# Kernel optimization log

Measured on AMD Instinct MI355X. Metric: run time of the kernel, lower is better.

The kernel has to match this reference:

```python
import jax, jax.numpy as jnp
import numpy as np

TEMPERATURE = 8.0  # sqrt(d_k) with d_k = 64
EPS = 1e-8


def setup_inputs() -> dict:
    key = jax.random.key(0)
    kq, kk, kv, km = jax.random.split(key, 4)
    B, L, D = 16, 2048, 64
    q = jax.random.normal(kq, (B, L, D), dtype=jnp.float32)
    k = jax.random.normal(kk, (B, L, D), dtype=jnp.float32)
    v = jax.random.normal(kv, (B, L, D), dtype=jnp.float32)
    # True entries are zeroed out AFTER softmax (post-softmax masking)
    mask = jax.random.randint(km, (B, L, L), 0, 2).astype(jnp.bool_)
    return {"q": q, "k": k, "v": v, "mask": mask}


def reference(q, k, v, mask):
    # attn scores: [B, Lq, Lk]
    attn = jnp.einsum("bqd,bkd->bqk", q, k) / TEMPERATURE
    attn = jax.nn.softmax(attn, axis=2)
    # post-softmax masking followed by renormalization (breaks flash-attn fusion)
    attn = jnp.where(mask, 0.0, attn)
    attn = attn / (jnp.sum(attn, axis=2, keepdims=True) + EPS)
    # dropout is identity in eval/reference mode
    output = jnp.einsum("bqk,bkd->bqd", attn, v)
    return output, attn
```

## Files before the change

kernel.cpp:

```cpp
#include <hip/hip_runtime.h>

#define BATCH 16
#define LSEQ 2048
#define DIM 64
#define TQ 32
#define SSTRIDE 2056
#define EPSV 1e-8f
#define SCALE_LOG2E 0.18033688011112042f

typedef float f4 __attribute__((ext_vector_type(4)));
typedef _Float16 h4 __attribute__((ext_vector_type(4)));
typedef _Float16 h8 __attribute__((ext_vector_type(8)));
typedef int i4t __attribute__((ext_vector_type(4)));

__device__ inline h8 cvt_h8(f4 a, f4 b) {
    h8 r;
    r[0] = (_Float16)a[0]; r[1] = (_Float16)a[1];
    r[2] = (_Float16)a[2]; r[3] = (_Float16)a[3];
    r[4] = (_Float16)b[0]; r[5] = (_Float16)b[1];
    r[6] = (_Float16)b[2]; r[7] = (_Float16)b[3];
    return r;
}

__device__ inline float fast_exp2(float x) {
#if __has_builtin(__builtin_amdgcn_exp2f)
    return __builtin_amdgcn_exp2f(x);
#else
    return exp2f(x);
#endif
}

__device__ inline void lds_barrier() {
    asm volatile("s_waitcnt lgkmcnt(0)" ::: "memory");
    __builtin_amdgcn_s_barrier();
    __builtin_amdgcn_sched_barrier(0);
}

__global__ __launch_bounds__(256)
void cvt_k_kernel(const float* __restrict__ k, _Float16* __restrict__ kh) {
    const int idx = blockIdx.x * 256 + threadIdx.x;
    f4 v = ((const f4*)k)[idx];
    h4 h;
    #pragma unroll
    for (int e = 0; e < 4; ++e) h[e] = (_Float16)v[e];
    ((h4*)kh)[idx] = h;
}

__global__ __launch_bounds__(256)
void tr_v_kernel(const float* __restrict__ v, _Float16* __restrict__ vt) {
    __shared__ float tile[64][65];
    const int b = blockIdx.y, k0 = blockIdx.x * 64, t = threadIdx.x;
    const float* vb = v + ((size_t)b * LSEQ + k0) * DIM;
    #pragma unroll
    for (int p = 0; p < 4; ++p) {
        const int row = p * 16 + (t >> 4), c4 = (t & 15) * 4;
        f4 val = *(const f4*)(vb + row * DIM + c4);
        #pragma unroll
        for (int e = 0; e < 4; ++e) tile[row][c4 + e] = val[e];
    }
    __syncthreads();
    _Float16* vtb = vt + (size_t)b * DIM * LSEQ;
    #pragma unroll
    for (int p = 0; p < 4; ++p) {
        const int d = p * 16 + (t >> 4), k4 = (t & 15) * 4;
        h4 h;
        #pragma unroll
        for (int e = 0; e < 4; ++e) h[e] = (_Float16)tile[k4 + e][d];
        *(h4*)(vtb + (size_t)d * LSEQ + k0 + k4) = h;
    }
}

__global__ __launch_bounds__(1024, 4)
void attn_kernel(const float* __restrict__ q, const _Float16* __restrict__ kh,
                 const _Float16* __restrict__ vt, const int* __restrict__ mask,
                 float* __restrict__ out, float* __restrict__ attn)
{
    __shared__ __align__(16) _Float16 s_p[TQ][SSTRIDE];
    __shared__ float oacc[16][256];
    __shared__ float s_inv[TQ];

    const int b    = blockIdx.y;
    const int q0   = blockIdx.x * TQ;
    const int tid  = threadIdx.x;
    const int w    = tid >> 6;
    const int lane = tid & 63;
    const int quad = lane >> 4;
    const int m16  = lane & 15;

    const int* mrow0 = mask + ((size_t)b * LSEQ + q0 + 2 * w) * LSEQ;
    i4t mv0[8];
    #pragma unroll
    for (int j = 0; j < 8; ++j)
        mv0[j] = __builtin_nontemporal_load((const i4t*)(mrow0 + lane * 4 + 256 * j));

    const float* qrowA = q + ((size_t)b * LSEQ + q0 + m16) * DIM + quad * 8;
    const float* qrowB = qrowA + 16 * DIM;
    h8 aqA0 = cvt_h8(*(const f4*)(qrowA),      *(const f4*)(qrowA + 4));
    h8 aqA1 = cvt_h8(*(const f4*)(qrowA + 32), *(const f4*)(qrowA + 36));
    h8 aqB0 = cvt_h8(*(const f4*)(qrowB),      *(const f4*)(qrowB + 4));
    h8 aqB1 = cvt_h8(*(const f4*)(qrowB + 32), *(const f4*)(qrowB + 36));

    #pragma unroll 2
    for (int i = 0; i < 8; ++i) {
        const int c = w * 16 + i * 256;
        const _Float16* krow = kh + ((size_t)b * LSEQ + c + m16) * DIM + quad * 8;
        h8 bk0 = *(const h8*)(krow);
        h8 bk1 = *(const h8*)(krow + 32);
        f4 accA = {0.f, 0.f, 0.f, 0.f}, accB = {0.f, 0.f, 0.f, 0.f};
        accA = __builtin_amdgcn_mfma_f32_16x16x32_f16(aqA0, bk0, accA, 0, 0, 0);
        accA = __builtin_amdgcn_mfma_f32_16x16x32_f16(aqA1, bk1, accA, 0, 0, 0);
        accB = __builtin_amdgcn_mfma_f32_16x16x32_f16(aqB0, bk0, accB, 0, 0, 0);
        accB = __builtin_amdgcn_mfma_f32_16x16x32_f16(aqB1, bk1, accB, 0, 0, 0);
        #pragma unroll
        for (int r = 0; r < 4; ++r) {
            s_p[quad * 4 + r][c + m16]      = (_Float16)(accA[r] * SCALE_LOG2E);
            s_p[16 + quad * 4 + r][c + m16] = (_Float16)(accB[r] * SCALE_LOG2E);
        }
    }

    const int* mrow1 = mrow0 + LSEQ;
    i4t mv1[8];
    #pragma unroll
    for (int j = 0; j < 8; ++j)
        mv1[j] = __builtin_nontemporal_load((const i4t*)(mrow1 + lane * 4 + 256 * j));

    lds_barrier();

    float inv0 = 0.f, inv1 = 0.f;
    #pragma unroll
    for (int rr = 0; rr < 2; ++rr) {
        const int row = 2 * w + rr;
        float sa = 0.f, sk = 0.f;
        h4 pk[8];
        #pragma unroll
        for (int j = 0; j < 8; ++j) {
            h4 hv = *(const h4*)(&s_p[row][lane * 4 + 256 * j]);
            i4t m = rr ? mv1[j] : mv0[j];
            #pragma unroll
            for (int e = 0; e < 4; ++e) {
                float p = fast_exp2((float)hv[e]);
                sa += p;
                float pm = m[e] ? 0.f : p;
                sk += pm;
                pk[j][e] = (_Float16)pm;
            }
        }
        #pragma unroll
        for (int off = 32; off >= 1; off >>= 1) {
            sa += __shfl_xor(sa, off);
            sk += __shfl_xor(sk, off);
        }
        const float inv_d = 1.f / (sk + EPSV * sa);
        if (rr == 0) inv0 = inv_d; else inv1 = inv_d;
        if (lane == 0) s_inv[row] = inv_d;
        #pragma unroll
        for (int j = 0; j < 8; ++j)
            *(h4*)(&s_p[row][lane * 4 + 256 * j]) = pk[j];
    }

    lds_barrier();

    const int dt = w & 3;
    const int kq = w >> 2;
    const _Float16* vtr = vt + ((size_t)b * DIM + dt * 16 + m16) * LSEQ;
    f4 accA = {0.f, 0.f, 0.f, 0.f}, accB = {0.f, 0.f, 0.f, 0.f};
    #pragma unroll 4
    for (int kb = kq * 512; kb < kq * 512 + 512; kb += 32) {
        const int kk = kb + quad * 8;
        h8 bf  = *(const h8*)(vtr + kk);
        h8 afA = *(const h8*)(&s_p[m16][kk]);
        h8 afB = *(const h8*)(&s_p[16 + m16][kk]);
        accA = __builtin_amdgcn_mfma_f32_16x16x32_f16(afA, bf, accA, 0, 0, 0);
        accB = __builtin_amdgcn_mfma_f32_16x16x32_f16(afB, bf, accB, 0, 0, 0);
    }

    #pragma unroll
    for (int rr = 0; rr < 2; ++rr) {
        const int row = 2 * w + rr;
        const float ivd = rr ? inv1 : inv0;
        float* arow = attn + ((size_t)b * LSEQ + q0 + row) * LSEQ;
        #pragma unroll
        for (int j = 0; j < 8; ++j) {
            const int c = lane * 4 + 256 * j;
            h4 hv = *(const h4*)(&s_p[row][c]);
            f4 pv;
            #pragma unroll
            for (int e = 0; e < 4; ++e) pv[e] = ivd * (float)hv[e];
            __builtin_nontemporal_store(pv, (f4*)(&arow[c]));
        }
    }

    float* ob = out + ((size_t)b * LSEQ + q0) * DIM;

    #pragma unroll
    for (int r = 0; r < 4; ++r)
        oacc[w][(quad * 4 + r) * 16 + m16] = accA[r];
    lds_barrier();
    {
        const int row = tid >> 6;
        const int d   = tid & 63;
        const int dt2 = d >> 4, dc = d & 15;
        const int o   = row * 16 + dc;
        float vsum = oacc[dt2][o] + oacc[4 + dt2][o]
                   + oacc[8 + dt2][o] + oacc[12 + dt2][o];
        ob[row * DIM + d] = s_inv[row] * vsum;
    }
    lds_barrier();

    #pragma unroll
    for (int r = 0; r < 4; ++r)
        oacc[w][(quad * 4 + r) * 16 + m16] = accB[r];
    lds_barrier();
    {
        const int row = tid >> 6;
        const int d   = tid & 63;
        const int dt2 = d >> 4, dc = d & 15;
        const int o   = row * 16 + dc;
        float vsum = oacc[dt2][o] + oacc[4 + dt2][o]
                   + oacc[8 + dt2][o] + oacc[12 + dt2][o];
        ob[(16 + row) * DIM + d] = s_inv[16 + row] * vsum;
    }
}

__global__ __launch_bounds__(512, 4)
void attn_kernel_fb(const float* __restrict__ q, const float* __restrict__ k,
                    const float* __restrict__ v, const int* __restrict__ mask,
                    float* __restrict__ out, float* __restrict__ attn)
{
    __shared__ __align__(16) _Float16 s_p[16][SSTRIDE];
    __shared__ float oacc[8][16 * 16];
    __shared__ float s_inv[16];

    const int b = blockIdx.y, q0 = blockIdx.x * 16, tid = threadIdx.x;
    const int w = tid >> 6, lane = tid & 63, quad = lane >> 4, m16 = lane & 15;
    const float* kp = k + (size_t)b * LSEQ * DIM;
    const float* vp = v + (size_t)b * LSEQ * DIM;
    const float* qrow = q + ((size_t)b * LSEQ + q0 + m16) * DIM + quad * 8;
    h8 aq0 = cvt_h8(*(const f4*)(qrow),      *(const f4*)(qrow + 4));
    h8 aq1 = cvt_h8(*(const f4*)(qrow + 32), *(const f4*)(qrow + 36));

    for (int t = w; t < LSEQ / 16; t += 8) {
        const int c = t * 16;
        const float* krow = kp + (size_t)(c + m16) * DIM + quad * 8;
        h8 bk0 = cvt_h8(*(const f4*)(krow),      *(const f4*)(krow + 4));
        h8 bk1 = cvt_h8(*(const f4*)(krow + 32), *(const f4*)(krow + 36));
        f4 acc = {0.f, 0.f, 0.f, 0.f};
        acc = __builtin_amdgcn_mfma_f32_16x16x32_f16(aq0, bk0, acc, 0, 0, 0);
        acc = __builtin_amdgcn_mfma_f32_16x16x32_f16(aq1, bk1, acc, 0, 0, 0);
        #pragma unroll
        for (int r = 0; r < 4; ++r)
            s_p[quad * 4 + r][c + m16] = (_Float16)(acc[r] * 0.125f);
    }
    __syncthreads();

    #pragma unroll
    for (int rr = 0; rr < 2; ++rr) {
        const int row = 2 * w + rr;
        const int* mrow = mask + ((size_t)b * LSEQ + q0 + row) * LSEQ;
        i4t mv[8];
        #pragma unroll
        for (int j = 0; j < 8; ++j)
            mv[j] = __builtin_nontemporal_load((const i4t*)(mrow + lane * 4 + 256 * j));
        float sa = 0.f, sk = 0.f;
        h4 pk[8];
        #pragma unroll
        for (int j = 0; j < 8; ++j) {
            h4 hv = *(const h4*)(&s_p[row][lane * 4 + 256 * j]);
            #pragma unroll
            for (int e = 0; e < 4; ++e) {
                float p = __expf((float)hv[e]);
                sa += p;
                float pm = mv[j][e] ? 0.f : p;
                sk += pm;
                pk[j][e] = (_Float16)pm;
            }
        }
        #pragma unroll
        for (int off = 32; off >= 1; off >>= 1) {
            sa += __shfl_xor(sa, off);
            sk += __shfl_xor(sk, off);
        }
        const float inv_d = 1.f / (sk + EPSV * sa);
        if (lane == 0) s_inv[row] = inv_d;
        float* arow = attn + ((size_t)b * LSEQ + q0 + row) * LSEQ;
        #pragma unroll
        for (int j = 0; j < 8; ++j) {
            const int c = lane * 4 + 256 * j;
            *(h4*)(&s_p[row][c]) = pk[j];
            f4 pv;
            #pragma unroll
            for (int e = 0; e < 4; ++e) pv[e] = inv_d * (float)pk[j][e];
            __builtin_nontemporal_store(pv, (f4*)(&arow[c]));
        }
    }
    __syncthreads();

    {
        const int dt = w >> 1, kh_ = w & 1;
        f4 acc = {0.f, 0.f, 0.f, 0.f};
        for (int kb0 = kh_ * 1024; kb0 < kh_ * 1024 + 1024; kb0 += 32) {
            const int kk = kb0 + quad * 8;
            h8 af = *(const h8*)(&s_p[m16][kk]);
            const float* vcol = vp + (size_t)kk * DIM + dt * 16 + m16;
            h8 bf;
            #pragma unroll
            for (int j = 0; j < 8; ++j) bf[j] = (_Float16)vcol[j * DIM];
            acc = __builtin_amdgcn_mfma_f32_16x16x32_f16(af, bf, acc, 0, 0, 0);
        }
        #pragma unroll
        for (int r = 0; r < 4; ++r)
            oacc[w][(quad * 4 + r) * 16 + m16] = acc[r];
    }
    __syncthreads();

    float* ob = out + ((size_t)b * LSEQ + q0) * DIM;
    #pragma unroll
    for (int it = 0; it < 2; ++it) {
        const int idx = tid + it * 512;
        const int row = idx >> 6, d = idx & 63;
        const int dt2 = d >> 4, dc = d & 15;
        ob[row * DIM + d] = s_inv[row] *
            (oacc[2 * dt2][row * 16 + dc] + oacc[2 * dt2 + 1][row * 16 + dc]);
    }
}

extern "C" void kernel_launch(void* const* d_in, const int* in_sizes, int n_in,
                              void* d_out, int out_size, void* d_ws, size_t ws_size,
                              hipStream_t stream) {
    const float* q = (const float*)d_in[0];
    const float* k = (const float*)d_in[1];
    const float* v = (const float*)d_in[2];
    const int* mask = (const int*)d_in[3];
    float* out = (float*)d_out;
    float* attn = out + (size_t)BATCH * LSEQ * DIM;

    const size_t kv_elems = (size_t)BATCH * LSEQ * DIM;
    if (ws_size >= kv_elems * 2 * sizeof(_Float16)) {
        _Float16* kh = (_Float16*)d_ws;
        _Float16* vt = kh + kv_elems;
        cvt_k_kernel<<<kv_elems / 4 / 256, 256, 0, stream>>>(k, kh);
        tr_v_kernel<<<dim3(LSEQ / 64, BATCH), 256, 0, stream>>>(v, vt);
        attn_kernel<<<dim3(LSEQ / TQ, BATCH), 1024, 0, stream>>>(q, kh, vt, mask, out, attn);
    } else {
        attn_kernel_fb<<<dim3(LSEQ / 16, BATCH), 512, 0, stream>>>(q, k, v, mask, out, attn);
    }
}
```

Baseline: 499.7 us.

## Process four query tiles per block with mask/Q prefetch; fuse K/V prep kernels

The attention kernel now loops over four consecutive 32-row query tiles per block. The grid shrinks to a quarter of its former size, so there is about one block per CU. While the PV MFMA loop and the attn-row stores for the current tile run, the next tile's mask rows and Q fragments are loaded into registers, so global mask latency overlaps with compute and stores. The K fp16 conversion and the V transpose are merged into one prep kernel to remove a launch. The risk is less parallelism to hide latency, since there are fewer blocks and the loop is serial, and higher register pressure from the prefetched mask arrays.

```diff
diff --git a/kernel.cpp b/kernel.cpp
--- a/kernel.cpp
+++ b/kernel.cpp
@@ -37,19 +37,24 @@
 }
 
 __global__ __launch_bounds__(256)
-void cvt_k_kernel(const float* __restrict__ k, _Float16* __restrict__ kh) {
-    const int idx = blockIdx.x * 256 + threadIdx.x;
-    f4 v = ((const f4*)k)[idx];
-    h4 h;
-    #pragma unroll
-    for (int e = 0; e < 4; ++e) h[e] = (_Float16)v[e];
-    ((h4*)kh)[idx] = h;
-}
-
-__global__ __launch_bounds__(256)
-void tr_v_kernel(const float* __restrict__ v, _Float16* __restrict__ vt) {
+void prep_kernel(const float* __restrict__ k, const float* __restrict__ v,
+                 _Float16* __restrict__ kh, _Float16* __restrict__ vt) {
     __shared__ float tile[64][65];
     const int b = blockIdx.y, k0 = blockIdx.x * 64, t = threadIdx.x;
+
+    {
+        const f4* kb = (const f4*)(k + ((size_t)b * LSEQ + k0) * DIM);
+        h4* khb = (h4*)(kh + ((size_t)b * LSEQ + k0) * DIM);
+        #pragma unroll
+        for (int p = 0; p < 4; ++p) {
+            f4 val = kb[t + 256 * p];
+            h4 h;
+            #pragma unroll
+            for (int e = 0; e < 4; ++e) h[e] = (_Float16)val[e];
+            khb[t + 256 * p] = h;
+        }
+    }
+
     const float* vb = v + ((size_t)b * LSEQ + k0) * DIM;
     #pragma unroll
     for (int p = 0; p < 4; ++p) {
@@ -80,145 +85,168 @@
     __shared__ float s_inv[TQ];
 
     const int b    = blockIdx.y;
-    const int q0   = blockIdx.x * TQ;
     const int tid  = threadIdx.x;
     const int w    = tid >> 6;
     const int lane = tid & 63;
     const int quad = lane >> 4;
     const int m16  = lane & 15;
 
-    const int* mrow0 = mask + ((size_t)b * LSEQ + q0 + 2 * w) * LSEQ;
-    i4t mv0[8];
-    #pragma unroll
-    for (int j = 0; j < 8; ++j)
-        mv0[j] = __builtin_nontemporal_load((const i4t*)(mrow0 + lane * 4 + 256 * j));
-
-    const float* qrowA = q + ((size_t)b * LSEQ + q0 + m16) * DIM + quad * 8;
-    const float* qrowB = qrowA + 16 * DIM;
-    h8 aqA0 = cvt_h8(*(const f4*)(qrowA),      *(const f4*)(qrowA + 4));
-    h8 aqA1 = cvt_h8(*(const f4*)(qrowA + 32), *(const f4*)(qrowA + 36));
-    h8 aqB0 = cvt_h8(*(const f4*)(qrowB),      *(const f4*)(qrowB + 4));
-    h8 aqB1 = cvt_h8(*(const f4*)(qrowB + 32), *(const f4*)(qrowB + 36));
-
-    #pragma unroll 2
-    for (int i = 0; i < 8; ++i) {
-        const int c = w * 16 + i * 256;
-        const _Float16* krow = kh + ((size_t)b * LSEQ + c + m16) * DIM + quad * 8;
-        h8 bk0 = *(const h8*)(krow);
-        h8 bk1 = *(const h8*)(krow + 32);
-        f4 accA = {0.f, 0.f, 0.f, 0.f}, accB = {0.f, 0.f, 0.f, 0.f};
-        accA = __builtin_amdgcn_mfma_f32_16x16x32_f16(aqA0, bk0, accA, 0, 0, 0);
-        accA = __builtin_amdgcn_mfma_f32_16x16x32_f16(aqA1, bk1, accA, 0, 0, 0);
-        accB = __builtin_amdgcn_mfma_f32_16x16x32_f16(aqB0, bk0, accB, 0, 0, 0);
-        accB = __builtin_amdgcn_mfma_f32_16x16x32_f16(aqB1, bk1, accB, 0, 0, 0);
-        #pragma unroll
-        for (int r = 0; r < 4; ++r) {
-            s_p[quad * 4 + r][c + m16]      = (_Float16)(accA[r] * SCALE_LOG2E);
-            s_p[16 + quad * 4 + r][c + m16] = (_Float16)(accB[r] * SCALE_LOG2E);
-        }
-    }
-
-    const int* mrow1 = mrow0 + LSEQ;
-    i4t mv1[8];
-    #pragma unroll
-    for (int j = 0; j < 8; ++j)
-        mv1[j] = __builtin_nontemporal_load((const i4t*)(mrow1 + lane * 4 + 256 * j));
-
-    lds_barrier();
-
-    float inv0 = 0.f, inv1 = 0.f;
-    #pragma unroll
-    for (int rr = 0; rr < 2; ++rr) {
-        const int row = 2 * w + rr;
-        float sa = 0.f, sk = 0.f;
-        h4 pk[8];
+    const _Float16* khb   = kh   + (size_t)b * LSEQ * DIM;
+    const _Float16* vtb   = vt   + (size_t)b * DIM * LSEQ;
+    const int*      mb    = mask + (size_t)b * LSEQ * LSEQ;
+    const float*    qb    = q    + (size_t)b * LSEQ * DIM;
+    float*          outb  = out  + (size_t)b * LSEQ * DIM;
+    float*          attnb = attn + (size_t)b * LSEQ * LSEQ;
+
+    int q0 = blockIdx.x * (4 * TQ);
+
+    i4t mv0[8], mv1[8];
+    {
+        const int* mr0 = mb + (size_t)(q0 + 2 * w) * LSEQ + lane * 4;
+        const int* mr1 = mr0 + LSEQ;
         #pragma unroll
         for (int j = 0; j < 8; ++j) {
-            h4 hv = *(const h4*)(&s_p[row][lane * 4 + 256 * j]);
-            i4t m = rr ? mv1[j] : mv0[j];
-            #pragma unroll
-            for (int e = 0; e < 4; ++e) {
-                float p = fast_exp2((float)hv[e]);
-                sa += p;
-                float pm = m[e] ? 0.f : p;
-                sk += pm;
-                pk[j][e] = (_Float16)pm;
-            }
-        }
-        #pragma unroll
-        for (int off = 32; off >= 1; off >>= 1) {
-            sa += __shfl_xor(sa, off);
-            sk += __shfl_xor(sk, off);
-        }
-        const float inv_d = 1.f / (sk + EPSV * sa);
-        if (rr == 0) inv0 = inv_d; else inv1 = inv_d;
-        if (lane == 0) s_inv[row] = inv_d;
-        #pragma unroll
-        for (int j = 0; j < 8; ++j)
-            *(h4*)(&s_p[row][lane * 4 + 256 * j]) = pk[j];
-    }
-
-    lds_barrier();
-
-    const int dt = w & 3;
-    const int kq = w >> 2;
-    const _Float16* vtr = vt + ((size_t)b * DIM + dt * 16 + m16) * LSEQ;
-    f4 accA = {0.f, 0.f, 0.f, 0.f}, accB = {0.f, 0.f, 0.f, 0.f};
-    #pragma unroll 4
-    for (int kb = kq * 512; kb < kq * 512 + 512; kb += 32) {
-        const int kk = kb + quad * 8;
-        h8 bf  = *(const h8*)(vtr + kk);
-        h8 afA = *(const h8*)(&s_p[m16][kk]);
-        h8 afB = *(const h8*)(&s_p[16 + m16][kk]);
-        accA = __builtin_amdgcn_mfma_f32_16x16x32_f16(afA, bf, accA, 0, 0, 0);
-        accB = __builtin_amdgcn_mfma_f32_16x16x32_f16(afB, bf, accB, 0, 0, 0);
-    }
-
-    #pragma unroll
-    for (int rr = 0; rr < 2; ++rr) {
-        const int row = 2 * w + rr;
-        const float ivd = rr ? inv1 : inv0;
-        float* arow = attn + ((size_t)b * LSEQ + q0 + row) * LSEQ;
-        #pragma unroll
-        for (int j = 0; j < 8; ++j) {
-            const int c = lane * 4 + 256 * j;
-            h4 hv = *(const h4*)(&s_p[row][c]);
-            f4 pv;
-            #pragma unroll
-            for (int e = 0; e < 4; ++e) pv[e] = ivd * (float)hv[e];
-            __builtin_nontemporal_store(pv, (f4*)(&arow[c]));
-        }
-    }
-
-    float* ob = out + ((size_t)b * LSEQ + q0) * DIM;
-
-    #pragma unroll
-    for (int r = 0; r < 4; ++r)
-        oacc[w][(quad * 4 + r) * 16 + m16] = accA[r];
-    lds_barrier();
+            mv0[j] = __builtin_nontemporal_load((const i4t*)(mr0 + 256 * j));
+            mv1[j] = __builtin_nontemporal_load((const i4t*)(mr1 + 256 * j));
+        }
+    }
+    h8 aqA0, aqA1, aqB0, aqB1;
     {
-        const int row = tid >> 6;
-        const int d   = tid & 63;
-        const int dt2 = d >> 4, dc = d & 15;
-        const int o   = row * 16 + dc;
-        float vsum = oacc[dt2][o] + oacc[4 + dt2][o]
-                   + oacc[8 + dt2][o] + oacc[12 + dt2][o];
-        ob[row * DIM + d] = s_inv[row] * vsum;
-    }
-    lds_barrier();
-
-    #pragma unroll
-    for (int r = 0; r < 4; ++r)
-        oacc[w][(quad * 4 + r) * 16 + m16] = accB[r];
-    lds_barrier();
-    {
-        const int row = tid >> 6;
-        const int d   = tid & 63;
-        const int dt2 = d >> 4, dc = d & 15;
-        const int o   = row * 16 + dc;
-        float vsum = oacc[dt2][o] + oacc[4 + dt2][o]
-                   + oacc[8 + dt2][o] + oacc[12 + dt2][o];
-        ob[(16 + row) * DIM + d] = s_inv[16 + row] * vsum;
+        const float* qrowA = qb + (size_t)(q0 + m16) * DIM + quad * 8;
+        const float* qrowB = qrowA + 16 * DIM;
+        aqA0 = cvt_h8(*(const f4*)(qrowA),      *(const f4*)(qrowA + 4));
+        aqA1 = cvt_h8(*(const f4*)(qrowA + 32), *(const f4*)(qrowA + 36));
+        aqB0 = cvt_h8(*(const f4*)(qrowB),      *(const f4*)(qrowB + 4));
+        aqB1 = cvt_h8(*(const f4*)(qrowB + 32), *(const f4*)(qrowB + 36));
+    }
+
+    for (int it = 0; it < 4; ++it, q0 += TQ) {
+        #pragma unroll 2
+        for (int i = 0; i < 8; ++i) {
+            const int c = w * 16 + i * 256;
+            const _Float16* krow = khb + (size_t)(c + m16) * DIM + quad * 8;
+            h8 bk0 = *(const h8*)(krow);
+            h8 bk1 = *(const h8*)(krow + 32);
+            f4 accA = {0.f, 0.f, 0.f, 0.f}, accB = {0.f, 0.f, 0.f, 0.f};
+            accA = __builtin_amdgcn_mfma_f32_16x16x32_f16(aqA0, bk0, accA, 0, 0, 0);
+            accA = __builtin_amdgcn_mfma_f32_16x16x32_f16(aqA1, bk1, accA, 0, 0, 0);
+            accB = __builtin_amdgcn_mfma_f32_16x16x32_f16(aqB0, bk0, accB, 0, 0, 0);
+            accB = __builtin_amdgcn_mfma_f32_16x16x32_f16(aqB1, bk1, accB, 0, 0, 0);
+            #pragma unroll
+            for (int r = 0; r < 4; ++r) {
+                s_p[quad * 4 + r][c + m16]      = (_Float16)(accA[r] * SCALE_LOG2E);
+                s_p[16 + quad * 4 + r][c + m16] = (_Float16)(accB[r] * SCALE_LOG2E);
+            }
+        }
+        lds_barrier();
+
+        float inv0 = 0.f, inv1 = 0.f;
+        #pragma unroll
+        for (int rr = 0; rr < 2; ++rr) {
+            const int row = 2 * w + rr;
+            float sa = 0.f, sk = 0.f;
+            h4 pk[8];
+            #pragma unroll
+            for (int j = 0; j < 8; ++j) {
+                h4 hv = *(const h4*)(&s_p[row][lane * 4 + 256 * j]);
+                i4t m = rr ? mv1[j] : mv0[j];
+                #pragma unroll
+                for (int e = 0; e < 4; ++e) {
+                    float p = fast_exp2((float)hv[e]);
+                    sa += p;
+                    float pm = m[e] ? 0.f : p;
+                    sk += pm;
+                    pk[j][e] = (_Float16)pm;
+                }
+            }
+            #pragma unroll
+            for (int off = 32; off >= 1; off >>= 1) {
+                sa += __shfl_xor(sa, off);
+                sk += __shfl_xor(sk, off);
+            }
+            const float inv_d = 1.f / (sk + EPSV * sa);
+            if (rr == 0) inv0 = inv_d; else inv1 = inv_d;
+            if (lane == 0) s_inv[row] = inv_d;
+            #pragma unroll
+            for (int j = 0; j < 8; ++j)
+                *(h4*)(&s_p[row][lane * 4 + 256 * j]) = pk[j];
+        }
+        lds_barrier();
+
+        const int dt = w & 3;
+        const int kq = w >> 2;
+        const _Float16* vtr = vtb + (size_t)(dt * 16 + m16) * LSEQ;
+        f4 eA = {0.f, 0.f, 0.f, 0.f}, eB = {0.f, 0.f, 0.f, 0.f};
+        #pragma unroll 4
+        for (int kb = kq * 512; kb < kq * 512 + 512; kb += 32) {
+            const int kk = kb + quad * 8;
+            h8 bf  = *(const h8*)(vtr + kk);
+            h8 afA = *(const h8*)(&s_p[m16][kk]);
+            h8 afB = *(const h8*)(&s_p[16 + m16][kk]);
+            eA = __builtin_amdgcn_mfma_f32_16x16x32_f16(afA, bf, eA, 0, 0, 0);
+            eB = __builtin_amdgcn_mfma_f32_16x16x32_f16(afB, bf, eB, 0, 0, 0);
+        }
+
+        if (it < 3) {
+            const int q0n = q0 + TQ;
+            const int* mr0 = mb + (size_t)(q0n + 2 * w) * LSEQ + lane * 4;
+            const int* mr1 = mr0 + LSEQ;
+            #pragma unroll
+            for (int j = 0; j < 8; ++j) {
+                mv0[j] = __builtin_nontemporal_load((const i4t*)(mr0 + 256 * j));
+                mv1[j] = __builtin_nontemporal_load((const i4t*)(mr1 + 256 * j));
+            }
+            const float* qrowA = qb + (size_t)(q0n + m16) * DIM + quad * 8;
+            const float* qrowB = qrowA + 16 * DIM;
+            aqA0 = cvt_h8(*(const f4*)(qrowA),      *(const f4*)(qrowA + 4));
+            aqA1 = cvt_h8(*(const f4*)(qrowA + 32), *(const f4*)(qrowA + 36));
+            aqB0 = cvt_h8(*(const f4*)(qrowB),      *(const f4*)(qrowB + 4));
+            aqB1 = cvt_h8(*(const f4*)(qrowB + 32), *(const f4*)(qrowB + 36));
+        }
+
+        #pragma unroll
+        for (int rr = 0; rr < 2; ++rr) {
+            const int row = 2 * w + rr;
+            const float ivd = rr ? inv1 : inv0;
+            float* arow = attnb + (size_t)(q0 + row) * LSEQ;
+            #pragma unroll
+            for (int j = 0; j < 8; ++j) {
+                const int c = lane * 4 + 256 * j;
+                h4 hv = *(const h4*)(&s_p[row][c]);
+                f4 pv;
+                #pragma unroll
+                for (int e = 0; e < 4; ++e) pv[e] = ivd * (float)hv[e];
+                __builtin_nontemporal_store(pv, (f4*)(&arow[c]));
+            }
+        }
+
+        #pragma unroll
+        for (int r = 0; r < 4; ++r)
+            oacc[w][(quad * 4 + r) * 16 + m16] = eA[r];
+        lds_barrier();
+        {
+            const int row = tid >> 6;
+            const int d   = tid & 63;
+            const int dt2 = d >> 4, dc = d & 15;
+            const int o   = row * 16 + dc;
+            float vsum = oacc[dt2][o] + oacc[4 + dt2][o]
+                       + oacc[8 + dt2][o] + oacc[12 + dt2][o];
+            outb[(size_t)(q0 + row) * DIM + d] = s_inv[row] * vsum;
+        }
+        lds_barrier();
+        #pragma unroll
+        for (int r = 0; r < 4; ++r)
+            oacc[w][(quad * 4 + r) * 16 + m16] = eB[r];
+        lds_barrier();
+        {
+            const int row = tid >> 6;
+            const int d   = tid & 63;
+            const int dt2 = d >> 4, dc = d & 15;
+            const int o   = row * 16 + dc;
+            float vsum = oacc[dt2][o] + oacc[4 + dt2][o]
+                       + oacc[8 + dt2][o] + oacc[12 + dt2][o];
+            outb[(size_t)(q0 + 16 + row) * DIM + d] = s_inv[16 + row] * vsum;
+        }
     }
 }
 
@@ -338,9 +366,8 @@
     if (ws_size >= kv_elems * 2 * sizeof(_Float16)) {
         _Float16* kh = (_Float16*)d_ws;
         _Float16* vt = kh + kv_elems;
-        cvt_k_kernel<<<kv_elems / 4 / 256, 256, 0, stream>>>(k, kh);
-        tr_v_kernel<<<dim3(LSEQ / 64, BATCH), 256, 0, stream>>>(v, vt);
-        attn_kernel<<<dim3(LSEQ / TQ, BATCH), 1024, 0, stream>>>(q, kh, vt, mask, out, attn);
+        prep_kernel<<<dim3(LSEQ / 64, BATCH), 256, 0, stream>>>(k, v, kh, vt);
+        attn_kernel<<<dim3(LSEQ / (4 * TQ), BATCH), 1024, 0, stream>>>(q, kh, vt, mask, out, attn);
     } else {
         attn_kernel_fb<<<dim3(LSEQ / 16, BATCH), 512, 0, stream>>>(q, k, v, mask, out, attn);
     }
```

After: 543.8 us. 8.8% more time.

## Pack int mask into bitmask in prep kernel; attention reads bits

Applied to the files above, without the earlier changes.

Adds a prep kernel that streams the int32 mask and packs it into a 1-bit-per-element bitmask in workspace, fused with the K fp16 conversion and V transpose. The attention kernel then reads 32x less mask data and holds far fewer mask registers, so its main cost becomes the attn write. The full mask is still read once, plus an extra bitmask write and read. This path only runs when the workspace is large enough; otherwise a fused K/V prep kernel with the original attention kernel is used.

```diff
diff --git a/kernel.cpp b/kernel.cpp
--- a/kernel.cpp
+++ b/kernel.cpp
@@ -7,6 +7,7 @@
 #define SSTRIDE 2056
 #define EPSV 1e-8f
 #define SCALE_LOG2E 0.18033688011112042f
+#define NBM_BLOCKS 4096
 
 typedef float f4 __attribute__((ext_vector_type(4)));
 typedef _Float16 h4 __attribute__((ext_vector_type(4)));
@@ -36,20 +37,23 @@
     __builtin_amdgcn_sched_barrier(0);
 }
 
-__global__ __launch_bounds__(256)
-void cvt_k_kernel(const float* __restrict__ k, _Float16* __restrict__ kh) {
-    const int idx = blockIdx.x * 256 + threadIdx.x;
-    f4 v = ((const f4*)k)[idx];
-    h4 h;
-    #pragma unroll
-    for (int e = 0; e < 4; ++e) h[e] = (_Float16)v[e];
-    ((h4*)kh)[idx] = h;
-}
-
-__global__ __launch_bounds__(256)
-void tr_v_kernel(const float* __restrict__ v, _Float16* __restrict__ vt) {
-    __shared__ float tile[64][65];
-    const int b = blockIdx.y, k0 = blockIdx.x * 64, t = threadIdx.x;
+__device__ inline void kv_prep_body(const float* __restrict__ k,
+                                    const float* __restrict__ v,
+                                    _Float16* __restrict__ kh,
+                                    _Float16* __restrict__ vt,
+                                    float (*tile)[65], int b, int k0, int t) {
+    {
+        const f4* kb = (const f4*)(k + ((size_t)b * LSEQ + k0) * DIM);
+        h4* khb = (h4*)(kh + ((size_t)b * LSEQ + k0) * DIM);
+        #pragma unroll
+        for (int p = 0; p < 4; ++p) {
+            f4 val = kb[t + 256 * p];
+            h4 h;
+            #pragma unroll
+            for (int e = 0; e < 4; ++e) h[e] = (_Float16)val[e];
+            khb[t + 256 * p] = h;
+        }
+    }
     const float* vb = v + ((size_t)b * LSEQ + k0) * DIM;
     #pragma unroll
     for (int p = 0; p < 4; ++p) {
@@ -70,10 +74,51 @@
     }
 }
 
+__global__ __launch_bounds__(256)
+void pre_kernel(const int* __restrict__ m, const float* __restrict__ k,
+                const float* __restrict__ v, unsigned int* __restrict__ bm32,
+                _Float16* __restrict__ kh, _Float16* __restrict__ vt) {
+    __shared__ float tile[64][65];
+    const int t = threadIdx.x;
+    if (blockIdx.x < NBM_BLOCKS) {
+        const int gwave = ((blockIdx.x << 8) | t) >> 6;
+        const int lane  = t & 63;
+        const int l8    = lane & 7;
+        const size_t base0 = (size_t)gwave * 4096;
+        #pragma unroll 4
+        for (int i = 0; i < 16; ++i) {
+            const size_t f = base0 + i * 256 + lane * 4;
+            i4t mv = *(const i4t*)(m + f);
+            unsigned int nib = (unsigned)(mv[0] != 0)
+                             | ((unsigned)(mv[1] != 0) << 1)
+                             | ((unsigned)(mv[2] != 0) << 2)
+                             | ((unsigned)(mv[3] != 0) << 3);
+            unsigned int x = nib << (l8 * 4);
+            x |= __shfl_xor(x, 1);
+            x |= __shfl_xor(x, 2);
+            x |= __shfl_xor(x, 4);
+            if (l8 == 0) bm32[f >> 5] = x;
+        }
+    } else {
+        const int pb = blockIdx.x - NBM_BLOCKS;
+        const int b  = pb >> 5;
+        const int k0 = (pb & 31) * 64;
+        kv_prep_body(k, v, kh, vt, tile, b, k0, t);
+    }
+}
+
+__global__ __launch_bounds__(256)
+void prep_kernel(const float* __restrict__ k, const float* __restrict__ v,
+                 _Float16* __restrict__ kh, _Float16* __restrict__ vt) {
+    __shared__ float tile[64][65];
+    kv_prep_body(k, v, kh, vt, tile, blockIdx.y, blockIdx.x * 64, threadIdx.x);
+}
+
 __global__ __launch_bounds__(1024, 4)
-void attn_kernel(const float* __restrict__ q, const _Float16* __restrict__ kh,
-                 const _Float16* __restrict__ vt, const int* __restrict__ mask,
-                 float* __restrict__ out, float* __restrict__ attn)
+void attn_kernel_bm(const float* __restrict__ q, const _Float16* __restrict__ kh,
+                    const _Float16* __restrict__ vt,
+                    const unsigned int* __restrict__ bm32,
+                    float* __restrict__ out, float* __restrict__ attn)
 {
     __shared__ __align__(16) _Float16 s_p[TQ][SSTRIDE];
     __shared__ float oacc[16][256];
@@ -87,11 +132,14 @@
     const int quad = lane >> 4;
     const int m16  = lane & 15;
 
-    const int* mrow0 = mask + ((size_t)b * LSEQ + q0 + 2 * w) * LSEQ;
-    i4t mv0[8];
-    #pragma unroll
-    for (int j = 0; j < 8; ++j)
-        mv0[j] = __builtin_nontemporal_load((const i4t*)(mrow0 + lane * 4 + 256 * j));
+    const unsigned int* bmr0 =
+        bm32 + ((size_t)b * LSEQ + q0 + 2 * w) * (LSEQ / 32) + (lane >> 3);
+    unsigned int bw0[8], bw1[8];
+    #pragma unroll
+    for (int j = 0; j < 8; ++j) {
+        bw0[j] = bmr0[8 * j];
+        bw1[j] = bmr0[LSEQ / 32 + 8 * j];
+    }
 
     const float* qrowA = q + ((size_t)b * LSEQ + q0 + m16) * DIM + quad * 8;
     const float* qrowB = qrowA + 16 * DIM;
@@ -118,14 +166,13 @@
         }
     }
 
-    const int* mrow1 = mrow0 + LSEQ;
-    i4t mv1[8];
     #pragma unroll
     for (int j = 0; j < 8; ++j)
-        mv1[j] = __builtin_nontemporal_load((const i4t*)(mrow1 + lane * 4 + 256 * j));
-
-    lds_barrier();
-
+        asm volatile("" :: "v"(bw0[j]), "v"(bw1[j]));
+
+    lds_barrier();
+
+    const int shift = (lane & 7) * 4;
     float inv0 = 0.f, inv1 = 0.f;
     #pragma unroll
     for (int rr = 0; rr < 2; ++rr) {
@@ -135,12 +182,12 @@
         #pragma unroll
         for (int j = 0; j < 8; ++j) {
             h4 hv = *(const h4*)(&s_p[row][lane * 4 + 256 * j]);
-            i4t m = rr ? mv1[j] : mv0[j];
+            const unsigned int nib = ((rr ? bw1[j] : bw0[j]) >> shift) & 0xFu;
             #pragma unroll
             for (int e = 0; e < 4; ++e) {
                 float p = fast_exp2((float)hv[e]);
                 sa += p;
-                float pm = m[e] ? 0.f : p;
+                float pm = ((nib >> e) & 1u) ? 0.f : p;
                 sk += pm;
                 pk[j][e] = (_Float16)pm;
             }
@@ -163,15 +210,15 @@
     const int dt = w & 3;
     const int kq = w >> 2;
     const _Float16* vtr = vt + ((size_t)b * DIM + dt * 16 + m16) * LSEQ;
-    f4 accA = {0.f, 0.f, 0.f, 0.f}, accB = {0.f, 0.f, 0.f, 0.f};
+    f4 eA = {0.f, 0.f, 0.f, 0.f}, eB = {0.f, 0.f, 0.f, 0.f};
     #pragma unroll 4
     for (int kb = kq * 512; kb < kq * 512 + 512; kb += 32) {
         const int kk = kb + quad * 8;
         h8 bf  = *(const h8*)(vtr + kk);
         h8 afA = *(const h8*)(&s_p[m16][kk]);
         h8 afB = *(const h8*)(&s_p[16 + m16][kk]);
-        accA = __builtin_amdgcn_mfma_f32_16x16x32_f16(afA, bf, accA, 0, 0, 0);
-        accB = __builtin_amdgcn_mfma_f32_16x16x32_f16(afB, bf, accB, 0, 0, 0);
+        eA = __builtin_amdgcn_mfma_f32_16x16x32_f16(afA, bf, eA, 0, 0, 0);
+        eB = __builtin_amdgcn_mfma_f32_16x16x32_f16(afB, bf, eB, 0, 0, 0);
     }
 
     #pragma unroll
@@ -194,7 +241,7 @@
 
     #pragma unroll
     for (int r = 0; r < 4; ++r)
-        oacc[w][(quad * 4 + r) * 16 + m16] = accA[r];
+        oacc[w][(quad * 4 + r) * 16 + m16] = eA[r];
     lds_barrier();
     {
         const int row = tid >> 6;
@@ -209,7 +256,157 @@
 
     #pragma unroll
     for (int r = 0; r < 4; ++r)
-        oacc[w][(quad * 4 + r) * 16 + m16] = accB[r];
+        oacc[w][(quad * 4 + r) * 16 + m16] = eB[r];
+    lds_barrier();
+    {
+        const int row = tid >> 6;
+        const int d   = tid & 63;
+        const int dt2 = d >> 4, dc = d & 15;
+        const int o   = row * 16 + dc;
+        float vsum = oacc[dt2][o] + oacc[4 + dt2][o]
+                   + oacc[8 + dt2][o] + oacc[12 + dt2][o];
+        ob[(16 + row) * DIM + d] = s_inv[16 + row] * vsum;
+    }
+}
+
+__global__ __launch_bounds__(1024, 4)
+void attn_kernel(const float* __restrict__ q, const _Float16* __restrict__ kh,
+                 const _Float16* __restrict__ vt, const int* __restrict__ mask,
+                 float* __restrict__ out, float* __restrict__ attn)
+{
+    __shared__ __align__(16) _Float16 s_p[TQ][SSTRIDE];
+    __shared__ float oacc[16][256];
+    __shared__ float s_inv[TQ];
+
+    const int b    = blockIdx.y;
+    const int q0   = blockIdx.x * TQ;
+    const int tid  = threadIdx.x;
+    const int w    = tid >> 6;
+    const int lane = tid & 63;
+    const int quad = lane >> 4;
+    const int m16  = lane & 15;
+
+    const int* mrow0 = mask + ((size_t)b * LSEQ + q0 + 2 * w) * LSEQ;
+    i4t mv0[8];
+    #pragma unroll
+    for (int j = 0; j < 8; ++j)
+        mv0[j] = __builtin_nontemporal_load((const i4t*)(mrow0 + lane * 4 + 256 * j));
+
+    const float* qrowA = q + ((size_t)b * LSEQ + q0 + m16) * DIM + quad * 8;
+    const float* qrowB = qrowA + 16 * DIM;
+    h8 aqA0 = cvt_h8(*(const f4*)(qrowA),      *(const f4*)(qrowA + 4));
+    h8 aqA1 = cvt_h8(*(const f4*)(qrowA + 32), *(const f4*)(qrowA + 36));
+    h8 aqB0 = cvt_h8(*(const f4*)(qrowB),      *(const f4*)(qrowB + 4));
+    h8 aqB1 = cvt_h8(*(const f4*)(qrowB + 32), *(const f4*)(qrowB + 36));
+
+    #pragma unroll 2
+    for (int i = 0; i < 8; ++i) {
+        const int c = w * 16 + i * 256;
+        const _Float16* krow = kh + ((size_t)b * LSEQ + c + m16) * DIM + quad * 8;
+        h8 bk0 = *(const h8*)(krow);
+        h8 bk1 = *(const h8*)(krow + 32);
+        f4 accA = {0.f, 0.f, 0.f, 0.f}, accB = {0.f, 0.f, 0.f, 0.f};
+        accA = __builtin_amdgcn_mfma_f32_16x16x32_f16(aqA0, bk0, accA, 0, 0, 0);
+        accA = __builtin_amdgcn_mfma_f32_16x16x32_f16(aqA1, bk1, accA, 0, 0, 0);
+        accB = __builtin_amdgcn_mfma_f32_16x16x32_f16(aqB0, bk0, accB, 0, 0, 0);
+        accB = __builtin_amdgcn_mfma_f32_16x16x32_f16(aqB1, bk1, accB, 0, 0, 0);
+        #pragma unroll
+        for (int r = 0; r < 4; ++r) {
+            s_p[quad * 4 + r][c + m16]      = (_Float16)(accA[r] * SCALE_LOG2E);
+            s_p[16 + quad * 4 + r][c + m16] = (_Float16)(accB[r] * SCALE_LOG2E);
+        }
+    }
+
+    const int* mrow1 = mrow0 + LSEQ;
+    i4t mv1[8];
+    #pragma unroll
+    for (int j = 0; j < 8; ++j)
+        mv1[j] = __builtin_nontemporal_load((const i4t*)(mrow1 + lane * 4 + 256 * j));
+
+    lds_barrier();
+
+    float inv0 = 0.f, inv1 = 0.f;
+    #pragma unroll
+    for (int rr = 0; rr < 2; ++rr) {
+        const int row = 2 * w + rr;
+        float sa = 0.f, sk = 0.f;
+        h4 pk[8];
+        #pragma unroll
+        for (int j = 0; j < 8; ++j) {
+            h4 hv = *(const h4*)(&s_p[row][lane * 4 + 256 * j]);
+            i4t m = rr ? mv1[j] : mv0[j];
+            #pragma unroll
+            for (int e = 0; e < 4; ++e) {
+                float p = fast_exp2((float)hv[e]);
+                sa += p;
+                float pm = m[e] ? 0.f : p;
+                sk += pm;
+                pk[j][e] = (_Float16)pm;
+            }
+        }
+        #pragma unroll
+        for (int off = 32; off >= 1; off >>= 1) {
+            sa += __shfl_xor(sa, off);
+            sk += __shfl_xor(sk, off);
+        }
+        const float inv_d = 1.f / (sk + EPSV * sa);
+        if (rr == 0) inv0 = inv_d; else inv1 = inv_d;
+        if (lane == 0) s_inv[row] = inv_d;
+        #pragma unroll
+        for (int j = 0; j < 8; ++j)
+            *(h4*)(&s_p[row][lane * 4 + 256 * j]) = pk[j];
+    }
+
+    lds_barrier();
+
+    const int dt = w & 3;
+    const int kq = w >> 2;
+    const _Float16* vtr = vt + ((size_t)b * DIM + dt * 16 + m16) * LSEQ;
+    f4 eA = {0.f, 0.f, 0.f, 0.f}, eB = {0.f, 0.f, 0.f, 0.f};
+    #pragma unroll 4
+    for (int kb = kq * 512; kb < kq * 512 + 512; kb += 32) {
+        const int kk = kb + quad * 8;
+        h8 bf  = *(const h8*)(vtr + kk);
+        h8 afA = *(const h8*)(&s_p[m16][kk]);
+        h8 afB = *(const h8*)(&s_p[16 + m16][kk]);
+        eA = __builtin_amdgcn_mfma_f32_16x16x32_f16(afA, bf, eA, 0, 0, 0);
+        eB = __builtin_amdgcn_mfma_f32_16x16x32_f16(afB, bf, eB, 0, 0, 0);
+    }
+
+    #pragma unroll
+    for (int rr = 0; rr < 2; ++rr) {
+        const int row = 2 * w + rr;
+        const float ivd = rr ? inv1 : inv0;
+        float* arow = attn + ((size_t)b * LSEQ + q0 + row) * LSEQ;
+        #pragma unroll
+        for (int j = 0; j < 8; ++j) {
+            const int c = lane * 4 + 256 * j;
+            h4 hv = *(const h4*)(&s_p[row][c]);
+            f4 pv;
+            #pragma unroll
+            for (int e = 0; e < 4; ++e) pv[e] = ivd * (float)hv[e];
+            __builtin_nontemporal_store(pv, (f4*)(&arow[c]));
+        }
+    }
+
+    float* ob = out + ((size_t)b * LSEQ + q0) * DIM;
+    #pragma unroll
+    for (int r = 0; r < 4; ++r)
+        oacc[w][(quad * 4 + r) * 16 + m16] = eA[r];
+    lds_barrier();
+    {
+        const int row = tid >> 6;
+        const int d   = tid & 63;
+        const int dt2 = d >> 4, dc = d & 15;
+        const int o   = row * 16 + dc;
+        float vsum = oacc[dt2][o] + oacc[4 + dt2][o]
+                   + oacc[8 + dt2][o] + oacc[12 + dt2][o];
+        ob[row * DIM + d] = s_inv[row] * vsum;
+    }
+    lds_barrier();
+    #pragma unroll
+    for (int r = 0; r < 4; ++r)
+        oacc[w][(quad * 4 + r) * 16 + m16] = eB[r];
     lds_barrier();
     {
         const int row = tid >> 6;
@@ -335,13 +532,25 @@
     float* attn = out + (size_t)BATCH * LSEQ * DIM;
 
     const size_t kv_elems = (size_t)BATCH * LSEQ * DIM;
-    if (ws_size >= kv_elems * 2 * sizeof(_Float16)) {
+    const size_t kv_bytes = kv_elems * sizeof(_Float16);
+    const size_t bm_bytes = (size_t)BATCH * LSEQ * LSEQ / 8;
+
+    if (ws_size >= bm_bytes + 2 * kv_bytes) {
+        unsigned int* bm = (unsigned int*)d_ws;
+        _Float16* kh = (_Float16*)((char*)d_ws + bm_bytes);
+        _Float16* vt = kh + kv_elems;
+        pre_kernel<<<NBM_BLOCKS + (LSEQ / 64) * BATCH, 256, 0, stream>>>(
+            mask, k, v, bm, kh, vt);
+        attn_kernel_bm<<<dim3(LSEQ / TQ, BATCH), 1024, 0, stream>>>(
+            q, kh, vt, bm, out, attn);
+    } else if (ws_size >= 2 * kv_bytes) {
         _Float16* kh = (_Float16*)d_ws;
         _Float16* vt = kh + kv_elems;
-        cvt_k_kernel<<<kv_elems / 4 / 256, 256, 0, stream>>>(k, kh);
-        tr_v_kernel<<<dim3(LSEQ / 64, BATCH), 256, 0, stream>>>(v, vt);
-        attn_kernel<<<dim3(LSEQ / TQ, BATCH), 1024, 0, stream>>>(q, kh, vt, mask, out, attn);
+        prep_kernel<<<dim3(LSEQ / 64, BATCH), 256, 0, stream>>>(k, v, kh, vt);
+        attn_kernel<<<dim3(LSEQ / TQ, BATCH), 1024, 0, stream>>>(
+            q, kh, vt, mask, out, attn);
     } else {
-        attn_kernel_fb<<<dim3(LSEQ / 16, BATCH), 512, 0, stream>>>(q, k, v, mask, out, attn);
-    }
-}
+        attn_kernel_fb<<<dim3(LSEQ / 16, BATCH), 512, 0, stream>>>(
+            q, k, v, mask, out, attn);
+    }
+}
```

Measured after the change: 550.7 us. 10.2% more time.

## Fuse exp and mask into QK MFMA epilogue and merge K/V prep kernels

Applied to the files above, without the earlier changes.

The exponentiation, post-softmax masking and row-sum accumulation now happen right after the QK MFMA, in the accumulator layout. Per-wave partial sums are reduced through shared memory. This removes a full LDS read-modify-write pass over the score tile, and the fp16 rounding of logits before exp. The mask is now read as scattered 4-byte loads in the MFMA layout (16-lane column groups across rows) instead of coalesced vector nontemporal loads, which may hurt memory efficiency on the dominant mask stream. The K conversion and V transpose kernels are merged into one launch.

```diff
diff --git a/kernel.cpp b/kernel.cpp
--- a/kernel.cpp
+++ b/kernel.cpp
@@ -37,19 +37,23 @@
 }
 
 __global__ __launch_bounds__(256)
-void cvt_k_kernel(const float* __restrict__ k, _Float16* __restrict__ kh) {
-    const int idx = blockIdx.x * 256 + threadIdx.x;
-    f4 v = ((const f4*)k)[idx];
-    h4 h;
-    #pragma unroll
-    for (int e = 0; e < 4; ++e) h[e] = (_Float16)v[e];
-    ((h4*)kh)[idx] = h;
-}
-
-__global__ __launch_bounds__(256)
-void tr_v_kernel(const float* __restrict__ v, _Float16* __restrict__ vt) {
+void prep_kernel(const float* __restrict__ k, const float* __restrict__ v,
+                 _Float16* __restrict__ kh, _Float16* __restrict__ vt) {
     __shared__ float tile[64][65];
     const int b = blockIdx.y, k0 = blockIdx.x * 64, t = threadIdx.x;
+
+    {
+        const f4* kb = (const f4*)(k + ((size_t)b * LSEQ + k0) * DIM);
+        h4* khb = (h4*)(kh + ((size_t)b * LSEQ + k0) * DIM);
+        #pragma unroll
+        for (int p = 0; p < 4; ++p) {
+            f4 val = kb[t + 256 * p];
+            h4 h;
+            #pragma unroll
+            for (int e = 0; e < 4; ++e) h[e] = (_Float16)val[e];
+            khb[t + 256 * p] = h;
+        }
+    }
     const float* vb = v + ((size_t)b * LSEQ + k0) * DIM;
     #pragma unroll
     for (int p = 0; p < 4; ++p) {
@@ -77,6 +81,8 @@
 {
     __shared__ __align__(16) _Float16 s_p[TQ][SSTRIDE];
     __shared__ float oacc[16][256];
+    __shared__ float s_psa[16][TQ];
+    __shared__ float s_psk[16][TQ];
     __shared__ float s_inv[TQ];
 
     const int b    = blockIdx.y;
@@ -87,12 +93,6 @@
     const int quad = lane >> 4;
     const int m16  = lane & 15;
 
-    const int* mrow0 = mask + ((size_t)b * LSEQ + q0 + 2 * w) * LSEQ;
-    i4t mv0[8];
-    #pragma unroll
-    for (int j = 0; j < 8; ++j)
-        mv0[j] = __builtin_nontemporal_load((const i4t*)(mrow0 + lane * 4 + 256 * j));
-
     const float* qrowA = q + ((size_t)b * LSEQ + q0 + m16) * DIM + quad * 8;
     const float* qrowB = qrowA + 16 * DIM;
     h8 aqA0 = cvt_h8(*(const f4*)(qrowA),      *(const f4*)(qrowA + 4));
@@ -100,12 +100,23 @@
     h8 aqB0 = cvt_h8(*(const f4*)(qrowB),      *(const f4*)(qrowB + 4));
     h8 aqB1 = cvt_h8(*(const f4*)(qrowB + 32), *(const f4*)(qrowB + 36));
 
+    const int* mbp = mask + ((size_t)b * LSEQ + q0) * LSEQ;
+
+    float saA[4] = {0.f, 0.f, 0.f, 0.f}, skA[4] = {0.f, 0.f, 0.f, 0.f};
+    float saB[4] = {0.f, 0.f, 0.f, 0.f}, skB[4] = {0.f, 0.f, 0.f, 0.f};
     #pragma unroll 2
     for (int i = 0; i < 8; ++i) {
         const int c = w * 16 + i * 256;
         const _Float16* krow = kh + ((size_t)b * LSEQ + c + m16) * DIM + quad * 8;
         h8 bk0 = *(const h8*)(krow);
         h8 bk1 = *(const h8*)(krow + 32);
+        const int* mc = mbp + c + m16;
+        int mA[4], mB[4];
+        #pragma unroll
+        for (int r = 0; r < 4; ++r) {
+            mA[r] = mc[(quad * 4 + r) * LSEQ];
+            mB[r] = mc[(16 + quad * 4 + r) * LSEQ];
+        }
         f4 accA = {0.f, 0.f, 0.f, 0.f}, accB = {0.f, 0.f, 0.f, 0.f};
         accA = __builtin_amdgcn_mfma_f32_16x16x32_f16(aqA0, bk0, accA, 0, 0, 0);
         accA = __builtin_amdgcn_mfma_f32_16x16x32_f16(aqA1, bk1, accA, 0, 0, 0);
@@ -113,71 +124,64 @@
         accB = __builtin_amdgcn_mfma_f32_16x16x32_f16(aqB1, bk1, accB, 0, 0, 0);
         #pragma unroll
         for (int r = 0; r < 4; ++r) {
-            s_p[quad * 4 + r][c + m16]      = (_Float16)(accA[r] * SCALE_LOG2E);
-            s_p[16 + quad * 4 + r][c + m16] = (_Float16)(accB[r] * SCALE_LOG2E);
-        }
-    }
-
-    const int* mrow1 = mrow0 + LSEQ;
-    i4t mv1[8];
-    #pragma unroll
-    for (int j = 0; j < 8; ++j)
-        mv1[j] = __builtin_nontemporal_load((const i4t*)(mrow1 + lane * 4 + 256 * j));
-
-    lds_barrier();
-
-    float inv0 = 0.f, inv1 = 0.f;
-    #pragma unroll
-    for (int rr = 0; rr < 2; ++rr) {
-        const int row = 2 * w + rr;
+            float pA = fast_exp2(accA[r] * SCALE_LOG2E);
+            float pB = fast_exp2(accB[r] * SCALE_LOG2E);
+            saA[r] += pA;  saB[r] += pB;
+            float pmA = mA[r] ? 0.f : pA;
+            float pmB = mB[r] ? 0.f : pB;
+            skA[r] += pmA; skB[r] += pmB;
+            s_p[quad * 4 + r][c + m16]      = (_Float16)pmA;
+            s_p[16 + quad * 4 + r][c + m16] = (_Float16)pmB;
+        }
+    }
+
+    #pragma unroll
+    for (int off = 1; off <= 8; off <<= 1) {
+        #pragma unroll
+        for (int r = 0; r < 4; ++r) {
+            saA[r] += __shfl_xor(saA[r], off);
+            skA[r] += __shfl_xor(skA[r], off);
+            saB[r] += __shfl_xor(saB[r], off);
+            skB[r] += __shfl_xor(skB[r], off);
+        }
+    }
+    if (m16 == 0) {
+        #pragma unroll
+        for (int r = 0; r < 4; ++r) {
+            s_psa[w][quad * 4 + r]      = saA[r];
+            s_psk[w][quad * 4 + r]      = skA[r];
+            s_psa[w][16 + quad * 4 + r] = saB[r];
+            s_psk[w][16 + quad * 4 + r] = skB[r];
+        }
+    }
+    lds_barrier();
+
+    if (tid < TQ) {
         float sa = 0.f, sk = 0.f;
-        h4 pk[8];
-        #pragma unroll
-        for (int j = 0; j < 8; ++j) {
-            h4 hv = *(const h4*)(&s_p[row][lane * 4 + 256 * j]);
-            i4t m = rr ? mv1[j] : mv0[j];
-            #pragma unroll
-            for (int e = 0; e < 4; ++e) {
-                float p = fast_exp2((float)hv[e]);
-                sa += p;
-                float pm = m[e] ? 0.f : p;
-                sk += pm;
-                pk[j][e] = (_Float16)pm;
-            }
-        }
-        #pragma unroll
-        for (int off = 32; off >= 1; off >>= 1) {
-            sa += __shfl_xor(sa, off);
-            sk += __shfl_xor(sk, off);
-        }
-        const float inv_d = 1.f / (sk + EPSV * sa);
-        if (rr == 0) inv0 = inv_d; else inv1 = inv_d;
-        if (lane == 0) s_inv[row] = inv_d;
-        #pragma unroll
-        for (int j = 0; j < 8; ++j)
-            *(h4*)(&s_p[row][lane * 4 + 256 * j]) = pk[j];
-    }
-
+        #pragma unroll
+        for (int ww = 0; ww < 16; ++ww) { sa += s_psa[ww][tid]; sk += s_psk[ww][tid]; }
+        s_inv[tid] = 1.f / (sk + EPSV * sa);
+    }
     lds_barrier();
 
     const int dt = w & 3;
     const int kq = w >> 2;
     const _Float16* vtr = vt + ((size_t)b * DIM + dt * 16 + m16) * LSEQ;
-    f4 accA = {0.f, 0.f, 0.f, 0.f}, accB = {0.f, 0.f, 0.f, 0.f};
+    f4 eA = {0.f, 0.f, 0.f, 0.f}, eB = {0.f, 0.f, 0.f, 0.f};
     #pragma unroll 4
     for (int kb = kq * 512; kb < kq * 512 + 512; kb += 32) {
         const int kk = kb + quad * 8;
         h8 bf  = *(const h8*)(vtr + kk);
         h8 afA = *(const h8*)(&s_p[m16][kk]);
         h8 afB = *(const h8*)(&s_p[16 + m16][kk]);
-        accA = __builtin_amdgcn_mfma_f32_16x16x32_f16(afA, bf, accA, 0, 0, 0);
-        accB = __builtin_amdgcn_mfma_f32_16x16x32_f16(afB, bf, accB, 0, 0, 0);
+        eA = __builtin_amdgcn_mfma_f32_16x16x32_f16(afA, bf, eA, 0, 0, 0);
+        eB = __builtin_amdgcn_mfma_f32_16x16x32_f16(afB, bf, eB, 0, 0, 0);
     }
 
     #pragma unroll
     for (int rr = 0; rr < 2; ++rr) {
         const int row = 2 * w + rr;
-        const float ivd = rr ? inv1 : inv0;
+        const float ivd = s_inv[row];
         float* arow = attn + ((size_t)b * LSEQ + q0 + row) * LSEQ;
         #pragma unroll
         for (int j = 0; j < 8; ++j) {
@@ -194,7 +198,7 @@
 
     #pragma unroll
     for (int r = 0; r < 4; ++r)
-        oacc[w][(quad * 4 + r) * 16 + m16] = accA[r];
+        oacc[w][(quad * 4 + r) * 16 + m16] = eA[r];
     lds_barrier();
     {
         const int row = tid >> 6;
@@ -209,7 +213,7 @@
 
     #pragma unroll
     for (int r = 0; r < 4; ++r)
-        oacc[w][(quad * 4 + r) * 16 + m16] = accB[r];
+        oacc[w][(quad * 4 + r) * 16 + m16] = eB[r];
     lds_barrier();
     {
         const int row = tid >> 6;
@@ -335,13 +339,16 @@
     float* attn = out + (size_t)BATCH * LSEQ * DIM;
 
     const size_t kv_elems = (size_t)BATCH * LSEQ * DIM;
-    if (ws_size >= kv_elems * 2 * sizeof(_Float16)) {
+    const size_t kv_bytes = kv_elems * sizeof(_Float16);
+
+    if (ws_size >= 2 * kv_bytes) {
         _Float16* kh = (_Float16*)d_ws;
         _Float16* vt = kh + kv_elems;
-        cvt_k_kernel<<<kv_elems / 4 / 256, 256, 0, stream>>>(k, kh);
-        tr_v_kernel<<<dim3(LSEQ / 64, BATCH), 256, 0, stream>>>(v, vt);
-        attn_kernel<<<dim3(LSEQ / TQ, BATCH), 1024, 0, stream>>>(q, kh, vt, mask, out, attn);
+        prep_kernel<<<dim3(LSEQ / 64, BATCH), 256, 0, stream>>>(k, v, kh, vt);
+        attn_kernel<<<dim3(LSEQ / TQ, BATCH), 1024, 0, stream>>>(
+            q, kh, vt, mask, out, attn);
     } else {
-        attn_kernel_fb<<<dim3(LSEQ / 16, BATCH), 512, 0, stream>>>(q, k, v, mask, out, attn);
-    }
-}
+        attn_kernel_fb<<<dim3(LSEQ / 16, BATCH), 512, 0, stream>>>(
+            q, k, v, mask, out, attn);
+    }
+}
```

After: 500.6 us. Within noise of the previous version (+0.2%).
